# Performance work log

Measured on AMD Instinct MI355X. Metric: run time of the kernel, lower is better.

## Reference

```python
import jax, jax.numpy as jnp
import numpy as np

EMBED_DIM = 1024
NUM_HEADS = 16
HEAD_DIM = EMBED_DIM // NUM_HEADS


def setup_inputs() -> dict:
    key = jax.random.key(0)
    kx, kw1, kb1, kw2, kb2 = jax.random.split(key, 5)
    B, T, C = 4, 2048, EMBED_DIM
    s = 1.0 / np.sqrt(C)
    return {
        "x": jax.random.normal(kx, (B, T, C), dtype=jnp.float32),
        "qkv_w": jax.random.uniform(kw1, (3 * C, C), jnp.float32, -s, s),
        "qkv_b": jax.random.uniform(kb1, (3 * C,), jnp.float32, -s, s),
        "out_w": jax.random.uniform(kw2, (C, C), jnp.float32, -s, s),
        "out_b": jax.random.uniform(kb2, (C,), jnp.float32, -s, s),
    }


def reference(x, qkv_w, qkv_b, out_w, out_b):
    B, T, C = x.shape
    H, D = NUM_HEADS, HEAD_DIM
    qkv = x @ qkv_w.T + qkv_b                      # [B,T,3C]
    qkv = qkv.reshape(B, T, 3, H, D)
    q = qkv[:, :, 0].transpose(0, 2, 1, 3)         # [B,H,T,D]
    k = qkv[:, :, 1].transpose(0, 2, 1, 3)
    v = qkv[:, :, 2].transpose(0, 2, 1, 3)
    att = jnp.einsum("bhqd,bhkd->bhqk", q, k) / jnp.sqrt(jnp.float32(D))
    causal = jnp.tril(jnp.ones((T, T), dtype=bool))
    att = jnp.where(causal, att, -jnp.inf)
    att = jax.nn.softmax(att, axis=-1)
    out = jnp.einsum("bhqk,bhkd->bhqd", att, v)    # [B,H,T,D]
    out = out.transpose(0, 2, 1, 3).reshape(B, T, C)
    return out @ out_w.T + out_b
```

## Files before the change

### kernel.cpp

```cpp
#include <hip/hip_runtime.h>
#include <stdint.h>

typedef _Float16 f16;
typedef _Float16 f16x2 __attribute__((ext_vector_type(2)));
typedef _Float16 f16x4 __attribute__((ext_vector_type(4)));
typedef _Float16 f16x8 __attribute__((ext_vector_type(8)));
typedef float f32x4 __attribute__((ext_vector_type(4)));
typedef float f32x16 __attribute__((ext_vector_type(16)));
typedef unsigned int u32;
typedef unsigned int u32x4 __attribute__((ext_vector_type(4)));
typedef int i32x2 __attribute__((ext_vector_type(2)));

#define LOG2E 1.44269504088896340736f

__device__ __forceinline__ f32x4 mfma_16x16x32(f16x8 a, f16x8 b, f32x4 c) {
    return __builtin_amdgcn_mfma_f32_16x16x32_f16(a, b, c, 0, 0, 0);
}
__device__ __forceinline__ f32x16 mfma_32x32x16(f16x8 a, f16x8 b, f32x16 c) {
    return __builtin_amdgcn_mfma_f32_32x32x16_f16(a, b, c, 0, 0, 0);
}

__device__ __forceinline__ void gload_lds16(const void* g, void* l) {
    __builtin_amdgcn_global_load_lds(
        (const __attribute__((address_space(1))) unsigned int*)g,
        (__attribute__((address_space(3))) unsigned int*)l, 16, 0, 0);
}

__device__ __forceinline__ f16x2 cvt_pk_f16(float a, float b) {
    return __builtin_bit_cast(f16x2, __builtin_amdgcn_cvt_pkrtz(a, b));
}

__device__ __forceinline__ void plswap_u32(u32& a, u32& b) {
    i32x2 r = __builtin_amdgcn_permlane32_swap((int)a, (int)b, false, false);
    a = (u32)r[0]; b = (u32)r[1];
}

__global__ void cast_f32_f16(const float* __restrict__ src, f16* __restrict__ dst, int n4) {
    int i = blockIdx.x * 256 + threadIdx.x;
    if (i >= n4) return;
    float4 v = reinterpret_cast<const float4*>(src)[i];
    f16x4 o;
    o[0] = (f16)v.x; o[1] = (f16)v.y; o[2] = (f16)v.z; o[3] = (f16)v.w;
    reinterpret_cast<f16x4*>(dst)[i] = o;
}

template<int MODE>
__global__ __launch_bounds__(256, 2)
void gemm_tn(const f16* __restrict__ A, const f16* __restrict__ W,
             const float* __restrict__ bias, void* __restrict__ outp,
             int M, int N, int K)
{
    __shared__ __align__(16) f16 As[2][128 * 32];
    __shared__ __align__(16) f16 Bs[2][128 * 32];

    const int lane = threadIdx.x & 63;
    const int wave = threadIdx.x >> 6;
    const int l15 = lane & 15, l4 = lane >> 4;

    const int nwg = (int)(gridDim.x * gridDim.y);
    int orig = (int)(blockIdx.y * gridDim.x + blockIdx.x);
    int cpx = nwg >> 3;
    int w = (orig & 7) * cpx + (orig >> 3);
    const int row0 = (w / (int)gridDim.x) * 128;
    const int col0 = (w % (int)gridDim.x) * 128;
    const int wr = wave >> 1, wc = wave & 1;

    f32x4 acc[4][4] = {};

    const int srow = lane >> 2;
    const int scol = (lane & 3) * 8;
    const int nk = K >> 5;

    #pragma unroll
    for (int it = 0; it < 2; ++it) {
        int chunk = it * 4 + wave;
        gload_lds16(A + (size_t)(row0 + chunk * 16 + srow) * K + scol, As[0] + chunk * 512);
        gload_lds16(W + (size_t)(col0 + chunk * 16 + srow) * K + scol, Bs[0] + chunk * 512);
    }
    __syncthreads();

    for (int i = 0; i < nk; ++i) {
        const int cur = i & 1;

        if (i + 1 < nk) {
            const int k1 = (i + 1) << 5;
            #pragma unroll
            for (int it = 0; it < 2; ++it) {
                int chunk = it * 4 + wave;
                gload_lds16(A + (size_t)(row0 + chunk * 16 + srow) * K + k1 + scol, As[cur ^ 1] + chunk * 512);
                gload_lds16(W + (size_t)(col0 + chunk * 16 + srow) * K + k1 + scol, Bs[cur ^ 1] + chunk * 512);
            }
        }

        f16x8 af[4], bf[4];
        #pragma unroll
        for (int m = 0; m < 4; ++m)
            af[m] = *reinterpret_cast<const f16x8*>(As[cur] + (wr * 64 + m * 16 + l15) * 32 + l4 * 8);
        #pragma unroll
        for (int n = 0; n < 4; ++n)
            bf[n] = *reinterpret_cast<const f16x8*>(Bs[cur] + (wc * 64 + n * 16 + l15) * 32 + l4 * 8);
        #pragma unroll
        for (int m = 0; m < 4; ++m)
            #pragma unroll
            for (int n = 0; n < 4; ++n)
                acc[m][n] = mfma_16x16x32(af[m], bf[n], acc[m][n]);

        __syncthreads();
    }

    if (MODE == 0) {
        f16* qb = (f16*)outp;
        const size_t HS = (size_t)64 * 2048 * 64;
        #pragma unroll
        for (int m = 0; m < 4; ++m) {
            int rbase = row0 + wr * 64 + m * 16 + l4 * 4;
            #pragma unroll
            for (int n = 0; n < 4; ++n) {
                int j = col0 + wc * 64 + n * 16 + l15;
                int which = j >> 10;
                int h = (j >> 6) & 15;
                int d = j & 63;
                float bj = bias[j];
                f16* base = qb + (size_t)which * HS;
                float scale = (which == 0) ? (0.125f * LOG2E) : 1.0f;
                #pragma unroll
                for (int r = 0; r < 4; ++r) {
                    int row = rbase + r;
                    int b = row >> 11, t = row & 2047;
                    size_t off = ((size_t)(b * 16 + h) * 2048 + t) * 64 + d;
                    base[off] = (f16)((acc[m][n][r] + bj) * scale);
                }
            }
        }
    } else {
        float* O = (float*)outp;
        #pragma unroll
        for (int m = 0; m < 4; ++m) {
            int rbase = row0 + wr * 64 + m * 16 + l4 * 4;
            #pragma unroll
            for (int n = 0; n < 4; ++n) {
                int j = col0 + wc * 64 + n * 16 + l15;
                float bj = bias[j];
                #pragma unroll
                for (int r = 0; r < 4; ++r)
                    O[(size_t)(rbase + r) * N + j] = acc[m][n][r] + bj;
            }
        }
    }
}

__global__ __launch_bounds__(256, 4)
void attn_kernel(const f16* __restrict__ qb, const f16* __restrict__ kb,
                 const f16* __restrict__ vb, f16* __restrict__ ob)
{
    __shared__ __align__(16) f16 Ks[2][4096];
    __shared__ __align__(16) f16 Vs[2][64][68];

    const int tid = (int)threadIdx.x;
    const int bh = (int)blockIdx.x;
    const int qblk = (int)gridDim.y - 1 - (int)blockIdx.y;
    const int lane = tid & 63;
    const int wave = tid >> 6;
    const int l31 = lane & 31;
    const int hi  = lane >> 5;
    const int q0 = qblk * 128;
    const int qw = q0 + wave * 32;

    const f16* Qp = qb + ((size_t)bh * 2048 + qw) * 64;
    f16x8 qf[4];
    #pragma unroll
    for (int ss = 0; ss < 4; ++ss)
        qf[ss] = *reinterpret_cast<const f16x8*>(Qp + l31 * 64 + ss * 16 + hi * 8);

    float Mr = -1e30f, Lr = 0.0f;
    f32x16 oacc[2] = {};

    const int ntiles = 2 * qblk + 2;
    const f16* Kbh = kb + (size_t)bh * 2048 * 64;
    const f16* Vbh = vb + (size_t)bh * 2048 * 64;

    f16x8 vld0, vld1;
    {
        #pragma unroll
        for (int it = 0; it < 2; ++it) {
            int c = it * 4 + wave;
            gload_lds16(Kbh + lane * 64 + c * 8, &Ks[0][0] + c * 512);
        }
        vld0 = *reinterpret_cast<const f16x8*>(Vbh + lane * 64 + (wave * 2 + 0) * 8);
        vld1 = *reinterpret_cast<const f16x8*>(Vbh + lane * 64 + (wave * 2 + 1) * 8);
    }

    for (int t = 0; t < ntiles; ++t) {
        const int cur = t & 1;
        const int kv0 = t * 64;

        #pragma unroll
        for (int it = 0; it < 2; ++it) {
            int dblk = wave * 2 + it;
            const f16x8 v = it ? vld1 : vld0;
            #pragma unroll
            for (int e = 0; e < 8; ++e)
                Vs[cur][dblk * 8 + e][lane] = v[e];
        }

        __syncthreads();

        {
            const int kvn = (t + 1 < ntiles) ? (t + 1) * 64 : t * 64;
            const f16* Ktn = Kbh + (size_t)kvn * 64;
            #pragma unroll
            for (int it = 0; it < 2; ++it) {
                int c = it * 4 + wave;
                gload_lds16(Ktn + lane * 64 + c * 8, &Ks[cur ^ 1][0] + c * 512);
            }
            const f16* Vtn = Vbh + (size_t)kvn * 64;
            vld0 = *reinterpret_cast<const f16x8*>(Vtn + lane * 64 + (wave * 2 + 0) * 8);
            vld1 = *reinterpret_cast<const f16x8*>(Vtn + lane * 64 + (wave * 2 + 1) * 8);
        }

        if (kv0 <= qw + 31) {
            const f16* Ksc = &Ks[cur][0];

            f32x16 s0 = {}, s1 = {};
            __builtin_amdgcn_s_setprio(1);
            #pragma unroll
            for (int ss = 0; ss < 4; ++ss) {
                f16x8 kf0 = *reinterpret_cast<const f16x8*>(Ksc + (2 * ss + hi) * 512 + l31 * 8);
                f16x8 kf1 = *reinterpret_cast<const f16x8*>(Ksc + (2 * ss + hi) * 512 + (32 + l31) * 8);
                s0 = mfma_32x32x16(kf0, qf[ss], s0);
                s1 = mfma_32x32x16(kf1, qf[ss], s1);
            }
            __builtin_amdgcn_s_setprio(0);

            if (kv0 + 63 > qw) {
                const int qg = qw + l31;
                #pragma unroll
                for (int r = 0; r < 16; ++r) {
                    int k0g = kv0 + (r & 3) + 8 * (r >> 2) + 4 * hi;
                    if (k0g > qg)      s0[r] = -1e30f;
                    if (k0g + 32 > qg) s1[r] = -1e30f;
                }
            }

            float t16[16];
            #pragma unroll
            for (int i = 0; i < 16; ++i) t16[i] = fmaxf(s0[i], s1[i]);
            #pragma unroll
            for (int st = 8; st > 0; st >>= 1)
                #pragma unroll
                for (int i = 0; i < st; ++i) t16[i] = fmaxf(t16[i], t16[i + st]);
            float mx = t16[0];
            mx = fmaxf(mx, __shfl_xor(mx, 32));

            if (__any(mx > Mr + 8.0f)) {
                float nm = fmaxf(Mr, mx);
                float alpha = exp2f(Mr - nm);
                Mr = nm; Lr *= alpha;
                float ar[16];
                #pragma unroll
                for (int r = 0; r < 16; ++r)
                    ar[r] = __shfl(alpha, (r & 3) + 8 * (r >> 2) + 4 * hi);
                #pragma unroll
                for (int r = 0; r < 16; ++r) { oacc[0][r] *= ar[r]; oacc[1][r] *= ar[r]; }
            }

            float e0[16], e1[16];
            #pragma unroll
            for (int r = 0; r < 16; ++r) {
                e0[r] = exp2f(s0[r] - Mr);
                e1[r] = exp2f(s1[r] - Mr);
            }
            float sm[16];
            #pragma unroll
            for (int i = 0; i < 16; ++i) sm[i] = e0[i] + e1[i];
            #pragma unroll
            for (int st = 8; st > 0; st >>= 1)
                #pragma unroll
                for (int i = 0; i < st; ++i) sm[i] += sm[i + st];
            float rs = sm[0];
            rs += __shfl_xor(rs, 32);
            Lr += rs;

            u32 cpk[2][8];
            #pragma unroll
            for (int B = 0; B < 4; ++B) {
                cpk[0][2 * B]     = __builtin_bit_cast(u32, __builtin_amdgcn_cvt_pkrtz(e0[4 * B],     e0[4 * B + 1]));
                cpk[0][2 * B + 1] = __builtin_bit_cast(u32, __builtin_amdgcn_cvt_pkrtz(e0[4 * B + 2], e0[4 * B + 3]));
                cpk[1][2 * B]     = __builtin_bit_cast(u32, __builtin_amdgcn_cvt_pkrtz(e1[4 * B],     e1[4 * B + 1]));
                cpk[1][2 * B + 1] = __builtin_bit_cast(u32, __builtin_amdgcn_cvt_pkrtz(e1[4 * B + 2], e1[4 * B + 3]));
            }

            __builtin_amdgcn_s_setprio(1);
            #pragma unroll
            for (int ss = 0; ss < 4; ++ss) {
                const int kbi = ss >> 1, qq = ss & 1;
                u32 a0 = cpk[kbi][4 * qq + 0], b0 = cpk[kbi][4 * qq + 2];
                u32 a1 = cpk[kbi][4 * qq + 1], b1 = cpk[kbi][4 * qq + 3];
                plswap_u32(a0, b0);
                plswap_u32(a1, b1);
                u32x4 up; up[0] = a0; up[1] = a1; up[2] = b0; up[3] = b1;
                f16x8 pa = __builtin_bit_cast(f16x8, up);
                #pragma unroll
                for (int db = 0; db < 2; ++db) {
                    const f16* vp = &Vs[cur][db * 32 + l31][16 * ss + 8 * hi];
                    f16x4 v0 = *reinterpret_cast<const f16x4*>(vp);
                    f16x4 v1 = *reinterpret_cast<const f16x4*>(vp + 4);
                    f16x8 vf = __builtin_shufflevector(v0, v1, 0, 1, 2, 3, 4, 5, 6, 7);
                    oacc[db] = mfma_32x32x16(pa, vf, oacc[db]);
                }
            }
            __builtin_amdgcn_s_setprio(0);
        }
    }

    float rcp = 1.0f / Lr;
    float rr[16];
    #pragma unroll
    for (int r = 0; r < 16; ++r)
        rr[r] = __shfl(rcp, (r & 3) + 8 * (r >> 2) + 4 * hi);

    const int b = bh >> 4, h = bh & 15;
    f16* O = ob + ((size_t)b * 2048 + qw) * 1024 + h * 64;
    #pragma unroll
    for (int db = 0; db < 2; ++db)
        #pragma unroll
        for (int r = 0; r < 16; ++r) {
            int q = (r & 3) + 8 * (r >> 2) + 4 * hi;
            O[(size_t)q * 1024 + db * 32 + l31] = (f16)(oacc[db][r] * rr[r]);
        }
}

extern "C" void kernel_launch(void* const* d_in, const int* in_sizes, int n_in,
                              void* d_out, int out_size, void* d_ws, size_t ws_size,
                              hipStream_t stream)
{
    const float* x    = (const float*)d_in[0];
    const float* qkvw = (const float*)d_in[1];
    const float* qkvb = (const float*)d_in[2];
    const float* outw = (const float*)d_in[3];
    const float* outb = (const float*)d_in[4];
    float* out = (float*)d_out;

    f16* x_h    = (f16*)d_ws;
    f16* qkvw_h = x_h + (size_t)8192 * 1024;
    f16* outw_h = qkvw_h + (size_t)3072 * 1024;
    f16* q_buf  = outw_h + (size_t)1024 * 1024;
    f16* att_o  = q_buf + (size_t)3 * 8388608;

    cast_f32_f16<<<8192, 256, 0, stream>>>(x, x_h, 2097152);
    cast_f32_f16<<<3072, 256, 0, stream>>>(qkvw, qkvw_h, 786432);
    cast_f32_f16<<<1024, 256, 0, stream>>>(outw, outw_h, 262144);

    gemm_tn<0><<<dim3(24, 64), 256, 0, stream>>>(x_h, qkvw_h, qkvb, q_buf, 8192, 3072, 1024);
    attn_kernel<<<dim3(64, 16), 256, 0, stream>>>(q_buf, q_buf + 8388608, q_buf + 2 * 8388608, att_o);
    gemm_tn<1><<<dim3(8, 64), 256, 0, stream>>>(att_o, outw_h, outb, out, 8192, 1024, 1024);
}
```

Measured before the change: 195.3 us.

## Double K-step depth in GEMM and KV tile size in attention kernel

The GEMM now stages 64-wide K slices instead of 32, halving the number of barriers and loop iterations per output tile while doubling LDS per buffer. The attention kernel processes 128 keys per outer iteration as two 64-key sub-tiles, halving synchronisations and prefetch rounds. This costs more LDS and registers (an extra V prefetch set), so the attention launch bound drops from 4 to 2 blocks per CU, which reduces occupancy and latency hiding.

Result: slower. 212.5 us (+8.8%).

```diff
diff --git a/kernel.cpp b/kernel.cpp
--- a/kernel.cpp
+++ b/kernel.cpp
@@ -26,10 +26,6 @@
         (__attribute__((address_space(3))) unsigned int*)l, 16, 0, 0);
 }
 
-__device__ __forceinline__ f16x2 cvt_pk_f16(float a, float b) {
-    return __builtin_bit_cast(f16x2, __builtin_amdgcn_cvt_pkrtz(a, b));
-}
-
 __device__ __forceinline__ void plswap_u32(u32& a, u32& b) {
     i32x2 r = __builtin_amdgcn_permlane32_swap((int)a, (int)b, false, false);
     a = (u32)r[0]; b = (u32)r[1];
@@ -50,11 +46,12 @@
              const float* __restrict__ bias, void* __restrict__ outp,
              int M, int N, int K)
 {
-    __shared__ __align__(16) f16 As[2][128 * 32];
-    __shared__ __align__(16) f16 Bs[2][128 * 32];
-
-    const int lane = threadIdx.x & 63;
-    const int wave = threadIdx.x >> 6;
+    __shared__ __align__(16) f16 As[2][128 * 64];
+    __shared__ __align__(16) f16 Bs[2][128 * 64];
+
+    const int tid = (int)threadIdx.x;
+    const int lane = tid & 63;
+    const int wave = tid >> 6;
     const int l15 = lane & 15, l4 = lane >> 4;
 
     const int nwg = (int)(gridDim.x * gridDim.y);
@@ -66,44 +63,50 @@
     const int wr = wave >> 1, wc = wave & 1;
 
     f32x4 acc[4][4] = {};
-
-    const int srow = lane >> 2;
-    const int scol = (lane & 3) * 8;
-    const int nk = K >> 5;
-
-    #pragma unroll
-    for (int it = 0; it < 2; ++it) {
-        int chunk = it * 4 + wave;
-        gload_lds16(A + (size_t)(row0 + chunk * 16 + srow) * K + scol, As[0] + chunk * 512);
-        gload_lds16(W + (size_t)(col0 + chunk * 16 + srow) * K + scol, Bs[0] + chunk * 512);
-    }
+    const int nk = K >> 6;
+
+    auto stage = [&](int buf, int k0) {
+        #pragma unroll
+        for (int it = 0; it < 4; ++it) {
+            int c = it * 256 + tid;
+            int row = c >> 3;
+            int col = (c & 7) * 8;
+            gload_lds16(A + (size_t)(row0 + row) * K + k0 + col, As[buf] + c * 8);
+        }
+        #pragma unroll
+        for (int it = 0; it < 4; ++it) {
+            int c = it * 256 + tid;
+            int row = c >> 3;
+            int col = (c & 7) * 8;
+            gload_lds16(W + (size_t)(col0 + row) * K + k0 + col, Bs[buf] + c * 8);
+        }
+    };
+
+    stage(0, 0);
     __syncthreads();
 
     for (int i = 0; i < nk; ++i) {
         const int cur = i & 1;
-
-        if (i + 1 < nk) {
-            const int k1 = (i + 1) << 5;
-            #pragma unroll
-            for (int it = 0; it < 2; ++it) {
-                int chunk = it * 4 + wave;
-                gload_lds16(A + (size_t)(row0 + chunk * 16 + srow) * K + k1 + scol, As[cur ^ 1] + chunk * 512);
-                gload_lds16(W + (size_t)(col0 + chunk * 16 + srow) * K + k1 + scol, Bs[cur ^ 1] + chunk * 512);
-            }
-        }
-
-        f16x8 af[4], bf[4];
+        if (i + 1 < nk) stage(cur ^ 1, (i + 1) << 6);
+
+        f16x8 af[4][2], bf[4][2];
         #pragma unroll
         for (int m = 0; m < 4; ++m)
-            af[m] = *reinterpret_cast<const f16x8*>(As[cur] + (wr * 64 + m * 16 + l15) * 32 + l4 * 8);
+            #pragma unroll
+            for (int kc = 0; kc < 2; ++kc)
+                af[m][kc] = *reinterpret_cast<const f16x8*>(As[cur] + (wr * 64 + m * 16 + l15) * 64 + kc * 32 + l4 * 8);
         #pragma unroll
         for (int n = 0; n < 4; ++n)
-            bf[n] = *reinterpret_cast<const f16x8*>(Bs[cur] + (wc * 64 + n * 16 + l15) * 32 + l4 * 8);
-        #pragma unroll
-        for (int m = 0; m < 4; ++m)
-            #pragma unroll
-            for (int n = 0; n < 4; ++n)
-                acc[m][n] = mfma_16x16x32(af[m], bf[n], acc[m][n]);
+            #pragma unroll
+            for (int kc = 0; kc < 2; ++kc)
+                bf[n][kc] = *reinterpret_cast<const f16x8*>(Bs[cur] + (wc * 64 + n * 16 + l15) * 64 + kc * 32 + l4 * 8);
+        #pragma unroll
+        for (int kc = 0; kc < 2; ++kc)
+            #pragma unroll
+            for (int m = 0; m < 4; ++m)
+                #pragma unroll
+                for (int n = 0; n < 4; ++n)
+                    acc[m][n] = mfma_16x16x32(af[m][kc], bf[n][kc], acc[m][n]);
 
         __syncthreads();
     }
@@ -149,12 +152,12 @@
     }
 }
 
-__global__ __launch_bounds__(256, 4)
+__global__ __launch_bounds__(256, 2)
 void attn_kernel(const f16* __restrict__ qb, const f16* __restrict__ kb,
                  const f16* __restrict__ vb, f16* __restrict__ ob)
 {
-    __shared__ __align__(16) f16 Ks[2][4096];
-    __shared__ __align__(16) f16 Vs[2][64][68];
+    __shared__ __align__(16) f16 Ks[2][2][4096];
+    __shared__ __align__(16) f16 Vs[2][2][64][68];
 
     const int tid = (int)threadIdx.x;
     const int bh = (int)blockIdx.x;
@@ -175,51 +178,65 @@
     float Mr = -1e30f, Lr = 0.0f;
     f32x16 oacc[2] = {};
 
-    const int ntiles = 2 * qblk + 2;
+    const int ntiles = qblk + 1;
     const f16* Kbh = kb + (size_t)bh * 2048 * 64;
     const f16* Vbh = vb + (size_t)bh * 2048 * 64;
 
-    f16x8 vld0, vld1;
+    f16x8 vld[2][2];
     {
         #pragma unroll
-        for (int it = 0; it < 2; ++it) {
-            int c = it * 4 + wave;
-            gload_lds16(Kbh + lane * 64 + c * 8, &Ks[0][0] + c * 512);
-        }
-        vld0 = *reinterpret_cast<const f16x8*>(Vbh + lane * 64 + (wave * 2 + 0) * 8);
-        vld1 = *reinterpret_cast<const f16x8*>(Vbh + lane * 64 + (wave * 2 + 1) * 8);
+        for (int sub = 0; sub < 2; ++sub) {
+            const f16* Ksub = Kbh + (size_t)sub * 64 * 64;
+            #pragma unroll
+            for (int it = 0; it < 2; ++it) {
+                int c = it * 4 + wave;
+                gload_lds16(Ksub + lane * 64 + c * 8, &Ks[0][sub][0] + c * 512);
+            }
+            const f16* Vsub = Vbh + (size_t)sub * 64 * 64;
+            vld[sub][0] = *reinterpret_cast<const f16x8*>(Vsub + lane * 64 + (wave * 2 + 0) * 8);
+            vld[sub][1] = *reinterpret_cast<const f16x8*>(Vsub + lane * 64 + (wave * 2 + 1) * 8);
+        }
     }
 
     for (int t = 0; t < ntiles; ++t) {
         const int cur = t & 1;
-        const int kv0 = t * 64;
-
-        #pragma unroll
-        for (int it = 0; it < 2; ++it) {
-            int dblk = wave * 2 + it;
-            const f16x8 v = it ? vld1 : vld0;
-            #pragma unroll
-            for (int e = 0; e < 8; ++e)
-                Vs[cur][dblk * 8 + e][lane] = v[e];
-        }
+        const int kv0 = t * 128;
+
+        #pragma unroll
+        for (int sub = 0; sub < 2; ++sub)
+            #pragma unroll
+            for (int it = 0; it < 2; ++it) {
+                int dblk = wave * 2 + it;
+                const f16x8 v = vld[sub][it];
+                #pragma unroll
+                for (int e = 0; e < 8; ++e)
+                    Vs[cur][sub][dblk * 8 + e][lane] = v[e];
+            }
 
         __syncthreads();
 
         {
-            const int kvn = (t + 1 < ntiles) ? (t + 1) * 64 : t * 64;
-            const f16* Ktn = Kbh + (size_t)kvn * 64;
-            #pragma unroll
-            for (int it = 0; it < 2; ++it) {
-                int c = it * 4 + wave;
-                gload_lds16(Ktn + lane * 64 + c * 8, &Ks[cur ^ 1][0] + c * 512);
-            }
-            const f16* Vtn = Vbh + (size_t)kvn * 64;
-            vld0 = *reinterpret_cast<const f16x8*>(Vtn + lane * 64 + (wave * 2 + 0) * 8);
-            vld1 = *reinterpret_cast<const f16x8*>(Vtn + lane * 64 + (wave * 2 + 1) * 8);
-        }
-
-        if (kv0 <= qw + 31) {
-            const f16* Ksc = &Ks[cur][0];
+            const int kvn = (t + 1 < ntiles) ? (t + 1) * 128 : t * 128;
+            #pragma unroll
+            for (int sub = 0; sub < 2; ++sub) {
+                const f16* Ksub = Kbh + (size_t)(kvn + sub * 64) * 64;
+                #pragma unroll
+                for (int it = 0; it < 2; ++it) {
+                    int c = it * 4 + wave;
+                    gload_lds16(Ksub + lane * 64 + c * 8, &Ks[cur ^ 1][sub][0] + c * 512);
+                }
+                const f16* Vsub = Vbh + (size_t)(kvn + sub * 64) * 64;
+                vld[sub][0] = *reinterpret_cast<const f16x8*>(Vsub + lane * 64 + (wave * 2 + 0) * 8);
+                vld[sub][1] = *reinterpret_cast<const f16x8*>(Vsub + lane * 64 + (wave * 2 + 1) * 8);
+            }
+        }
+
+        #pragma unroll
+        for (int sub = 0; sub < 2; ++sub) {
+            const int kv0s = kv0 + sub * 64;
+            if (kv0s > qw + 31) continue;
+
+            const f16* Ksc = &Ks[cur][sub][0];
 
             f32x16 s0 = {}, s1 = {};
             __builtin_amdgcn_s_setprio(1);
@@ -232,11 +249,11 @@
             }
             __builtin_amdgcn_s_setprio(0);
 
-            if (kv0 + 63 > qw) {
+            if (kv0s + 63 > qw) {
                 const int qg = qw + l31;
                 #pragma unroll
                 for (int r = 0; r < 16; ++r) {
-                    int k0g = kv0 + (r & 3) + 8 * (r >> 2) + 4 * hi;
+                    int k0g = kv0s + (r & 3) + 8 * (r >> 2) + 4 * hi;
                     if (k0g > qg)      s0[r] = -1e30f;
                     if (k0g + 32 > qg) s1[r] = -1e30f;
                 }
@@ -302,7 +319,7 @@
                 f16x8 pa = __builtin_bit_cast(f16x8, up);
                 #pragma unroll
                 for (int db = 0; db < 2; ++db) {
-                    const f16* vp = &Vs[cur][db * 32 + l31][16 * ss + 8 * hi];
+                    const f16* vp = &Vs[cur][sub][db * 32 + l31][16 * ss + 8 * hi];
                     f16x4 v0 = *reinterpret_cast<const f16x4*>(vp);
                     f16x4 v1 = *reinterpret_cast<const f16x4*>(vp + 4);
                     f16x8 vf = __builtin_shufflevector(v0, v1, 0, 1, 2, 3, 4, 5, 6, 7);
```
